# Kernel tuning notes

Measured on AMD Instinct MI355X. Metric: run time of the kernel, lower is better.

Reference implementation:

```python
import jax, jax.numpy as jnp
import numpy as np

D_MODEL = 768
N_HEADS = 12
CHUNK = 512
N_LM = 32
BATCH = 2
SEQ = 8192


def setup_inputs() -> dict:
    key = jax.random.key(0)
    ks = jax.random.split(key, 9)
    s = 1.0 / np.sqrt(D_MODEL)
    return {
        "x": jax.random.normal(ks[0], (BATCH, SEQ, D_MODEL), jnp.float32),
        "Wq": jax.random.normal(ks[1], (D_MODEL, D_MODEL), jnp.float32) * s,
        "bq": jax.random.normal(ks[2], (D_MODEL,), jnp.float32) * 0.01,
        "Wk": jax.random.normal(ks[3], (D_MODEL, D_MODEL), jnp.float32) * s,
        "bk": jax.random.normal(ks[4], (D_MODEL,), jnp.float32) * 0.01,
        "Wv": jax.random.normal(ks[5], (D_MODEL, D_MODEL), jnp.float32) * s,
        "bv": jax.random.normal(ks[6], (D_MODEL,), jnp.float32) * 0.01,
        "Wo": jax.random.normal(ks[7], (D_MODEL, D_MODEL), jnp.float32) * s,
        "bo": jax.random.normal(ks[8], (D_MODEL,), jnp.float32) * 0.01,
    }


def reference(x, Wq, bq, Wk, bk, Wv, bv, Wo, bo):
    B, S, D = x.shape
    H, hd = N_HEADS, D // N_HEADS
    scale = hd ** -0.5
    n_chunks = S // CHUNK  # SEQ chosen divisible by CHUNK -> no padding path

    # Global landmarks: mean-pool over N_LM evenly spaced segments
    seg = S // N_LM
    lm = x[:, : seg * N_LM, :].reshape(B, N_LM, seg, D).mean(axis=2)  # (B, L, D)

    # Q over local tokens only
    q = (x @ Wq.T + bq).reshape(B, n_chunks, CHUNK, H, hd)

    # K/V over [landmarks ++ local chunk]
    xc = x.reshape(B, n_chunks, CHUNK, D)
    lm_exp = jnp.broadcast_to(lm[:, None], (B, n_chunks, N_LM, D))
    kv = jnp.concatenate([lm_exp, xc], axis=2)  # (B, n_chunks, N_LM+CHUNK, D)
    k = (kv @ Wk.T + bk).reshape(B, n_chunks, N_LM + CHUNK, H, hd)
    v = (kv @ Wv.T + bv).reshape(B, n_chunks, N_LM + CHUNK, H, hd)

    attn = jnp.einsum("bnqhd,bnkhd->bnhqk", q, k) * scale
    attn = jax.nn.softmax(attn, axis=-1)  # dropout=0 (eval)
    out = jnp.einsum("bnhqk,bnkhd->bnqhd", attn, v).reshape(B, S, D)
    return out @ Wo.T + bo
```

## Files before the change

kernel.cpp:

```cpp
#include <hip/hip_runtime.h>
#include <cstdint>
#include <cstddef>

#define D_MODEL 768
#define N_HEADS 12
#define HEAD_DIM 64
#define CHUNK_SZ 512
#define N_LM 32
#define BATCH 2
#define SEQ 8192
#define N_CH 16
#define SEG 256
#define TOK (BATCH*SEQ)
#define MKV_PAD 16512
#define QSCALE 0.18033688011112042f
#define DEFER_THR 12.0f

typedef unsigned short u16;
typedef __attribute__((ext_vector_type(8))) __bf16 bf16x8;
typedef __attribute__((ext_vector_type(4))) float f32x4;

__device__ __forceinline__ u16 f2bf_rn(float f){
  union { __bf16 b; u16 u; } c; c.b = (__bf16)f; return c.u;
}

#define GLOAD_LDS16(gp, lp) \
  __builtin_amdgcn_global_load_lds((const __attribute__((address_space(1))) void*)(gp), \
                                   (__attribute__((address_space(3))) void*)(lp), 16, 0, 0)

__device__ __forceinline__ int xcd_remap(int bid, int nwg){
  int q = nwg >> 3, r = nwg & 7;
  int xcd = bid & 7, j = bid >> 3;
  return (xcd < r ? xcd*(q+1) : r*(q+1) + (xcd-r)*q) + j;
}

__global__ __launch_bounds__(256) void cvt4_kernel(
    const float* __restrict__ w0, const float* __restrict__ w1,
    const float* __restrict__ w2, const float* __restrict__ w3,
    u16* __restrict__ o0, u16* __restrict__ o1, u16* __restrict__ o2, u16* __restrict__ o3)
{
  const int n4 = D_MODEL*D_MODEL/4;
  int i = blockIdx.x*256 + threadIdx.x;
  int sel = i / n4, j = i - sel*n4;
  const float* s = sel==0 ? w0 : sel==1 ? w1 : sel==2 ? w2 : w3;
  u16* o = sel==0 ? o0 : sel==1 ? o1 : sel==2 ? o2 : o3;
  float4 v = reinterpret_cast<const float4*>(s)[j];
  ushort4 p; p.x=f2bf_rn(v.x); p.y=f2bf_rn(v.y); p.z=f2bf_rn(v.z); p.w=f2bf_rn(v.w);
  reinterpret_cast<ushort4*>(o)[j] = p;
}

__global__ void build_xcat_kernel(const float* __restrict__ x, u16* __restrict__ xcat){
  const int total4 = MKV_PAD * D_MODEL / 4;
  const int x4 = TOK * D_MODEL / 4;
  int stride = gridDim.x * blockDim.x;
  for (int i = blockIdx.x*blockDim.x + threadIdx.x; i < total4; i += stride){
    ushort4 o;
    if (i < x4){
      float4 v = reinterpret_cast<const float4*>(x)[i];
      o.x = f2bf_rn(v.x); o.y = f2bf_rn(v.y); o.z = f2bf_rn(v.z); o.w = f2bf_rn(v.w);
    } else { o.x = 0; o.y = 0; o.z = 0; o.w = 0; }
    reinterpret_cast<ushort4*>(xcat)[i] = o;
  }
}

__global__ __launch_bounds__(256) void lm_part_kernel(const float* __restrict__ x, float* __restrict__ lmp){
  int seg = blockIdx.x >> 3, sub = blockIdx.x & 7;
  int b = seg >> 5, l = seg & 31;
  const float* base = x + ((size_t)b*SEQ + (size_t)l*SEG + (size_t)sub*32) * D_MODEL;
  int d = threadIdx.x;
  float a0=0.f, a1=0.f, a2=0.f;
  for (int tt=0; tt<32; ++tt){
    const float* row = base + (size_t)tt*D_MODEL;
    a0 += row[d]; a1 += row[d+256]; a2 += row[d+512];
  }
  float* orow = lmp + (size_t)blockIdx.x * D_MODEL;
  orow[d] = a0; orow[d+256] = a1; orow[d+512] = a2;
}
__global__ __launch_bounds__(256) void lm_final_kernel(const float* __restrict__ lmp, u16* __restrict__ xcat){
  int seg = blockIdx.x;
  int d = threadIdx.x;
  float a0=0.f, a1=0.f, a2=0.f;
  #pragma unroll
  for (int i=0;i<8;i++){
    const float* p = lmp + ((size_t)seg*8 + i)*D_MODEL;
    a0 += p[d]; a1 += p[d+256]; a2 += p[d+512];
  }
  u16* orow = xcat + ((size_t)TOK + seg)*D_MODEL;
  const float inv = 1.f/(float)SEG;
  orow[d] = f2bf_rn(a0*inv); orow[d+256] = f2bf_rn(a1*inv); orow[d+512] = f2bf_rn(a2*inv);
}

#define GEMM_PROLOG                                                                \
  const int t = threadIdx.x;                                                       \
  const int lane = t & 63, wid = t >> 6;                                           \
  const int wr = wid >> 1, wc = wid & 1;                                           \
  const int lr = lane & 15, lg = lane >> 4;

#define GEMM_MAINLOOP(Aptr, Bptr)                                                  \
  __shared__ u16 As[128*64];                                                       \
  __shared__ u16 Bs[128*64];                                                       \
  const int srow = lane >> 3, scol = (lane & 7) << 3;                              \
  const u16* ga = (Aptr) + (row0 + srow)*(size_t)D_MODEL + scol;                   \
  const u16* gb = (Bptr) + ((size_t)col0 + srow)*(size_t)D_MODEL + scol;           \
  f32x4 acc[4][4];                                                                 \
  _Pragma("unroll") for (int m=0;m<4;m++)                                          \
    _Pragma("unroll") for (int n=0;n<4;n++) acc[m][n] = f32x4{0.f,0.f,0.f,0.f};    \
  for (int ko = 0; ko < D_MODEL; ko += 64){                                        \
    _Pragma("unroll") for (int i=0;i<4;i++){                                       \
      int chunk = wid*4 + i;                                                       \
      GLOAD_LDS16(ga + (size_t)chunk*8*D_MODEL + ko, As + chunk*512);              \
      GLOAD_LDS16(gb + (size_t)chunk*8*D_MODEL + ko, Bs + chunk*512);              \
    }                                                                              \
    __syncthreads();                                                               \
    _Pragma("unroll") for (int kk=0;kk<2;kk++){                                    \
      bf16x8 af[4], bv[4];                                                         \
      _Pragma("unroll") for (int m=0;m<4;m++)                                      \
        af[m] = *reinterpret_cast<const bf16x8*>(&As[(wr*64 + m*16 + lr)*64 + kk*32 + lg*8]); \
      _Pragma("unroll") for (int n=0;n<4;n++)                                      \
        bv[n] = *reinterpret_cast<const bf16x8*>(&Bs[(wc*64 + n*16 + lr)*64 + kk*32 + lg*8]); \
      _Pragma("unroll") for (int m=0;m<4;m++)                                      \
        _Pragma("unroll") for (int n=0;n<4;n++)                                    \
          acc[m][n] = __builtin_amdgcn_mfma_f32_16x16x32_bf16(af[m], bv[n], acc[m][n], 0, 0, 0); \
    }                                                                              \
    __syncthreads();                                                               \
  }

template<int OUT_F32, int BIAS_ROW, int ROWFAST, int NFAST>
__global__ __launch_bounds__(256) void gemm_bt_kernel(
    const u16* __restrict__ A, const u16* __restrict__ Bt,
    const float* __restrict__ bias, void* __restrict__ Cout, int ldc, float scale)
{
  int g = xcd_remap(blockIdx.x, gridDim.x);
  int rowt, colt;
  if (ROWFAST){ rowt = g % NFAST; colt = g / NFAST; }
  else        { colt = g % NFAST; rowt = g / NFAST; }
  const size_t row0 = (size_t)rowt * 128;
  const int col0 = colt * 128;
  GEMM_PROLOG
  GEMM_MAINLOOP(A, Bt)
  #pragma unroll
  for (int m=0;m<4;m++){
    #pragma unroll
    for (int n=0;n<4;n++){
      const int col = col0 + wc*64 + n*16 + lr;
      const float bcol = BIAS_ROW ? 0.f : bias[col];
      #pragma unroll
      for (int e=0;e<4;e++){
        size_t row = row0 + wr*64 + m*16 + lg*4 + e;
        float b = BIAS_ROW ? bias[row] : bcol;
        float val = (acc[m][n][e] + b) * scale;
        if (OUT_F32) reinterpret_cast<float*>(Cout)[row*(size_t)ldc + col] = val;
        else         reinterpret_cast<u16*>(Cout)[row*(size_t)ldc + col] = f2bf_rn(val);
      }
    }
  }
}

__global__ __launch_bounds__(256) void gemm_qk_kernel(
    const u16* __restrict__ A, const u16* __restrict__ Wqk,
    const float* __restrict__ bq, const float* __restrict__ bk,
    u16* __restrict__ Qb, u16* __restrict__ Kb)
{
  int g = xcd_remap(blockIdx.x, gridDim.x);
  int colt = g % 12, rowt = g / 12;
  const size_t row0 = (size_t)rowt * 128;
  const int col0 = colt * 128;
  GEMM_PROLOG
  GEMM_MAINLOOP(A, Wqk)
  const bool isk = col0 >= 768;
  const float scale = isk ? 1.f : QSCALE;
  u16* dst = isk ? Kb : Qb;
  #pragma unroll
  for (int m=0;m<4;m++){
    #pragma unroll
    for (int n=0;n<4;n++){
      const int col = col0 + wc*64 + n*16 + lr;
      const int ocol = isk ? col - 768 : col;
      const float b = isk ? bk[ocol] : bq[ocol];
      #pragma unroll
      for (int e=0;e<4;e++){
        size_t row = row0 + wr*64 + m*16 + lg*4 + e;
        if (isk || row < TOK){
          float val = (acc[m][n][e] + b) * scale;
          dst[row*D_MODEL + ocol] = f2bf_rn(val);
        }
      }
    }
  }
}

template<int NK>
__device__ __forceinline__ void attn_compute(
    int lr, int lg,
    const u16 (* __restrict__ Ks)[72], const u16 (* __restrict__ Vs)[72],
    u16 (* __restrict__ Pw)[72],
    const bf16x8 (&qf)[2][2], float (&m_run)[2], float (&l_run)[2], f32x4 (&of)[2][4])
{
  constexpr int NCF = NK/16;
  constexpr int NKT = NK/32;

  f32x4 s2[2][NCF];
  #pragma unroll
  for (int c=0;c<NCF;c++){
    bf16x8 kf0 = *reinterpret_cast<const bf16x8*>(&Ks[c*16 + lr][lg*8]);
    bf16x8 kf1 = *reinterpret_cast<const bf16x8*>(&Ks[c*16 + lr][32 + lg*8]);
    #pragma unroll
    for (int r=0;r<2;r++){
      f32x4 s = f32x4{0.f,0.f,0.f,0.f};
      s = __builtin_amdgcn_mfma_f32_16x16x32_bf16(kf0, qf[r][0], s, 0,0,0);
      s = __builtin_amdgcn_mfma_f32_16x16x32_bf16(kf1, qf[r][1], s, 0,0,0);
      s2[r][c] = s;
    }
  }

  bf16x8 vf[NKT][4];
  #pragma unroll
  for (int kt=0;kt<NKT;kt++)
    #pragma unroll
    for (int c=0;c<4;c++)
      vf[kt][c] = *reinterpret_cast<const bf16x8*>(&Vs[c*16 + lr][kt*32 + lg*8]);

  #pragma unroll
  for (int r=0;r<2;r++){
    float tm = s2[r][0][0];
    #pragma unroll
    for (int c=0;c<NCF;c++)
      #pragma unroll
      for (int e=0;e<4;e++) tm = fmaxf(tm, s2[r][c][e]);
    tm = fmaxf(tm, __shfl_xor(tm, 16, 64));
    tm = fmaxf(tm, __shfl_xor(tm, 32, 64));
    if (!__all(tm - m_run[r] <= DEFER_THR)){
      float mnew = fmaxf(m_run[r], tm);
      float al = exp2f(m_run[r] - mnew);
      m_run[r] = mnew;
      l_run[r] *= al;
      #pragma unroll
      for (int c=0;c<4;c++)
        #pragma unroll
        for (int e=0;e<4;e++) of[r][c][e] *= al;
    }
    float ts = 0.f;
    #pragma unroll
    for (int c=0;c<NCF;c++)
      #pragma unroll
      for (int e=0;e<4;e++){
        float p = exp2f(s2[r][c][e] - m_run[r]);
        s2[r][c][e] = p;
        ts += p;
      }
    ts += __shfl_xor(ts, 16, 64);
    ts += __shfl_xor(ts, 32, 64);
    l_run[r] += ts;

    #pragma unroll
    for (int c=0;c<NCF;c++){
      ushort4 pk;
      pk.x = f2bf_rn(s2[r][c][0]); pk.y = f2bf_rn(s2[r][c][1]);
      pk.z = f2bf_rn(s2[r][c][2]); pk.w = f2bf_rn(s2[r][c][3]);
      *reinterpret_cast<ushort4*>(&Pw[lr][c*16 + lg*4]) = pk;
    }
    #pragma unroll
    for (int kt=0;kt<NKT;kt++){
      bf16x8 pf = *reinterpret_cast<const bf16x8*>(&Pw[lr][kt*32 + lg*8]);
      #pragma unroll
      for (int c=0;c<4;c++)
        of[r][c] = __builtin_amdgcn_mfma_f32_16x16x32_bf16(vf[kt][c], pf, of[r][c], 0,0,0);
    }
  }
}

__global__ __launch_bounds__(256) void attn_kernel(
    const u16* __restrict__ Qb, const u16* __restrict__ Kb,
    const u16* __restrict__ Vt, u16* __restrict__ AO)
{
  __shared__ u16 Ks[64][72];
  __shared__ u16 Vs[64][72];
  __shared__ u16 PwAll[4][16][72];

  const int t = threadIdx.x;
  const int lane = t & 63, w = t >> 6;
  const int lr = lane & 15, lg = lane >> 4;
  const int qt = blockIdx.x;
  const int h  = blockIdx.y;
  const int b  = blockIdx.z >> 4, ch = blockIdx.z & 15;
  const size_t tok0 = (size_t)b*SEQ + (size_t)ch*CHUNK_SZ + (size_t)qt*128;
  const size_t bch0 = (size_t)b*SEQ + (size_t)ch*CHUNK_SZ;
  u16 (* __restrict__ Pw)[72] = PwAll[w];

  bf16x8 qf[2][2];
  #pragma unroll
  for (int r=0;r<2;r++)
    #pragma unroll
    for (int kk=0;kk<2;kk++)
      qf[r][kk] = *reinterpret_cast<const bf16x8*>(
          &Qb[(tok0 + w*32 + r*16 + lr)*D_MODEL + (size_t)h*HEAD_DIM + kk*32 + lg*8]);

  float m_run[2] = {-INFINITY, -INFINITY};
  float l_run[2] = {0.f, 0.f};
  f32x4 of[2][4];
  #pragma unroll
  for (int r=0;r<2;r++)
    #pragma unroll
    for (int c=0;c<4;c++) of[r][c] = f32x4{0.f,0.f,0.f,0.f};

  {
    const size_t lmrow0 = (size_t)TOK + (size_t)b*N_LM;
    int key = t >> 3, dc = (t & 7) << 3;
    *reinterpret_cast<bf16x8*>(&Ks[key][dc]) = *reinterpret_cast<const bf16x8*>(
        &Kb[(lmrow0 + key)*D_MODEL + (size_t)h*HEAD_DIM + dc]);
    int d = t >> 2, kc = (t & 3) << 3;
    *reinterpret_cast<bf16x8*>(&Vs[d][kc]) = *reinterpret_cast<const bf16x8*>(
        &Vt[((size_t)h*HEAD_DIM + d)*MKV_PAD + lmrow0 + kc]);
    __syncthreads();
    attn_compute<32>(lr, lg, Ks, Vs, Pw, qf, m_run, l_run, of);
  }

  bf16x8 kreg[2], vreg[2];
  const int key0 = t >> 3, dc0 = (t & 7) << 3;
  const int d0 = t >> 3, kc0 = (t & 7) << 3;
  {
    size_t col0 = bch0;
    kreg[0] = *reinterpret_cast<const bf16x8*>(&Kb[(col0 + key0)*D_MODEL + (size_t)h*HEAD_DIM + dc0]);
    kreg[1] = *reinterpret_cast<const bf16x8*>(&Kb[(col0 + key0 + 32)*D_MODEL + (size_t)h*HEAD_DIM + dc0]);
    vreg[0] = *reinterpret_cast<const bf16x8*>(&Vt[((size_t)h*HEAD_DIM + d0)*MKV_PAD + col0 + kc0]);
    vreg[1] = *reinterpret_cast<const bf16x8*>(&Vt[((size_t)h*HEAD_DIM + d0 + 32)*MKV_PAD + col0 + kc0]);
  }
  for (int tl = 0; tl < 8; ++tl){
    __syncthreads();
    *reinterpret_cast<bf16x8*>(&Ks[key0][dc0])      = kreg[0];
    *reinterpret_cast<bf16x8*>(&Ks[key0 + 32][dc0]) = kreg[1];
    *reinterpret_cast<bf16x8*>(&Vs[d0][kc0])        = vreg[0];
    *reinterpret_cast<bf16x8*>(&Vs[d0 + 32][kc0])   = vreg[1];
    __syncthreads();
    if (tl < 7){
      size_t col0 = bch0 + (size_t)(tl+1)*64;
      kreg[0] = *reinterpret_cast<const bf16x8*>(&Kb[(col0 + key0)*D_MODEL + (size_t)h*HEAD_DIM + dc0]);
      kreg[1] = *reinterpret_cast<const bf16x8*>(&Kb[(col0 + key0 + 32)*D_MODEL + (size_t)h*HEAD_DIM + dc0]);
      vreg[0] = *reinterpret_cast<const bf16x8*>(&Vt[((size_t)h*HEAD_DIM + d0)*MKV_PAD + col0 + kc0]);
      vreg[1] = *reinterpret_cast<const bf16x8*>(&Vt[((size_t)h*HEAD_DIM + d0 + 32)*MKV_PAD + col0 + kc0]);
    }
    attn_compute<64>(lr, lg, Ks, Vs, Pw, qf, m_run, l_run, of);
  }

  #pragma unroll
  for (int r=0;r<2;r++){
    float inv = 1.f / l_run[r];
    size_t row = (tok0 + w*32 + r*16 + lr)*D_MODEL + (size_t)h*HEAD_DIM;
    #pragma unroll
    for (int c=0;c<4;c++){
      ushort4 pk;
      pk.x = f2bf_rn(of[r][c][0]*inv); pk.y = f2bf_rn(of[r][c][1]*inv);
      pk.z = f2bf_rn(of[r][c][2]*inv); pk.w = f2bf_rn(of[r][c][3]*inv);
      *reinterpret_cast<ushort4*>(&AO[row + c*16 + lg*4]) = pk;
    }
  }
}

extern "C" void kernel_launch(void* const* d_in, const int* in_sizes, int n_in,
                              void* d_out, int out_size, void* d_ws, size_t ws_size,
                              hipStream_t stream) {
  const float* x  = (const float*)d_in[0];
  const float* Wq = (const float*)d_in[1];
  const float* bq = (const float*)d_in[2];
  const float* Wk = (const float*)d_in[3];
  const float* bk = (const float*)d_in[4];
  const float* Wv = (const float*)d_in[5];
  const float* bv = (const float*)d_in[6];
  const float* Wo = (const float*)d_in[7];
  const float* bo = (const float*)d_in[8];
  float* out = (float*)d_out;

  const size_t XCAT_OFF = 0;
  const size_t Q_OFF    = 25362432;
  const size_t K_OFF    = 50528256;
  const size_t VT_OFF   = 75890688;
  const size_t AO_OFF   = 101253120;
  const size_t WQ_OFF   = 126418944;
  const size_t WK_OFF   = 127598592;
  const size_t WV_OFF   = 128778240;
  const size_t WO_OFF   = 129957888;
  const size_t TOTAL    = 131137536;
  if (ws_size < TOTAL) return;

  char* ws = (char*)d_ws;
  u16* xcat = (u16*)(ws + XCAT_OFF);
  u16* Qb   = (u16*)(ws + Q_OFF);
  u16* Kb   = (u16*)(ws + K_OFF);
  u16* Vt   = (u16*)(ws + VT_OFF);
  u16* AO   = (u16*)(ws + AO_OFF);
  float* lmp = (float*)(ws + AO_OFF);
  u16* wqkb = (u16*)(ws + WQ_OFF);
  u16* wkb  = (u16*)(ws + WK_OFF);
  u16* wvb  = (u16*)(ws + WV_OFF);
  u16* wob  = (u16*)(ws + WO_OFF);

  dim3 blk(256);
  cvt4_kernel<<<dim3(2304), blk, 0, stream>>>(Wq, Wk, Wv, Wo, wqkb, wkb, wvb, wob);
  build_xcat_kernel<<<dim3(4096), blk, 0, stream>>>(x, xcat);
  lm_part_kernel<<<dim3(512), blk, 0, stream>>>(x, lmp);
  lm_final_kernel<<<dim3(64), blk, 0, stream>>>(lmp, xcat);

  gemm_qk_kernel<<<dim3(1548), blk, 0, stream>>>(xcat, wqkb, bq, bk, Qb, Kb);
  gemm_bt_kernel<0,1,1,6><<<dim3(774), blk, 0, stream>>>(wvb, xcat, bv, (void*)Vt, MKV_PAD, 1.f);

  attn_kernel<<<dim3(4, 12, 32), blk, 0, stream>>>(Qb, Kb, Vt, AO);

  gemm_bt_kernel<1,0,0,6><<<dim3(768), blk, 0, stream>>>(AO, wob, bo, (void*)out, D_MODEL, 1.f);
}
```

Before: 268.6 us.

## Double-buffer GEMM LDS tiles and XOR-swizzle columns to avoid bank conflicts

The shared GEMM main loop now uses two LDS buffers for the A and B tiles. It prefetches the next K-slice with direct global-to-LDS loads while MFMAs consume the current one, which removes one barrier per iteration. Global source columns are XOR-permuted by row and LDS reads apply the matching swizzle, so 16-byte fragment reads spread across banks. Doubling LDS to 64KB per block may reduce occupancy, and a single barrier per step relies on async load ordering.

```diff
diff --git a/kernel.cpp b/kernel.cpp
--- a/kernel.cpp
+++ b/kernel.cpp
@@ -97,32 +97,49 @@
   const int lr = lane & 15, lg = lane >> 4;
 
 #define GEMM_MAINLOOP(Aptr, Bptr)                                                  \
-  __shared__ u16 As[128*64];                                                       \
-  __shared__ u16 Bs[128*64];                                                       \
-  const int srow = lane >> 3, scol = (lane & 7) << 3;                              \
-  const u16* ga = (Aptr) + (row0 + srow)*(size_t)D_MODEL + scol;                   \
-  const u16* gb = (Bptr) + ((size_t)col0 + srow)*(size_t)D_MODEL + scol;           \
+  __shared__ u16 As[2*128*64];                                                     \
+  __shared__ u16 Bs[2*128*64];                                                     \
+  const int srow = lane >> 3;                                                      \
+  const int scolx = (((lane & 7) ^ (lane >> 3)) << 3);   \
+  const u16* ga = (Aptr) + (row0 + srow)*(size_t)D_MODEL + scolx;                  \
+  const u16* gb = (Bptr) + ((size_t)col0 + srow)*(size_t)D_MODEL + scolx;          \
   f32x4 acc[4][4];                                                                 \
   _Pragma("unroll") for (int m=0;m<4;m++)                                          \
     _Pragma("unroll") for (int n=0;n<4;n++) acc[m][n] = f32x4{0.f,0.f,0.f,0.f};    \
-  for (int ko = 0; ko < D_MODEL; ko += 64){                                        \
+  {                                                                                \
     _Pragma("unroll") for (int i=0;i<4;i++){                                       \
       int chunk = wid*4 + i;                                                       \
-      GLOAD_LDS16(ga + (size_t)chunk*8*D_MODEL + ko, As + chunk*512);              \
-      GLOAD_LDS16(gb + (size_t)chunk*8*D_MODEL + ko, Bs + chunk*512);              \
+      GLOAD_LDS16(ga + (size_t)chunk*8*D_MODEL, As + chunk*512);                   \
+      GLOAD_LDS16(gb + (size_t)chunk*8*D_MODEL, Bs + chunk*512);                   \
     }                                                                              \
-    __syncthreads();                                                               \
+  }                                                                                \
+  __syncthreads();                                                                 \
+  int cur = 0;                                                                     \
+  const int rsw = (lr & 7) << 3;                                                   \
+  for (int ts = 0; ts < D_MODEL/64; ++ts){                                         \
+    if (ts < D_MODEL/64 - 1){                                                      \
+      int nb = (cur ^ 1) * 8192;                                                   \
+      _Pragma("unroll") for (int i=0;i<4;i++){                                     \
+        int chunk = wid*4 + i;                                                     \
+        GLOAD_LDS16(ga + (size_t)chunk*8*D_MODEL + (ts+1)*64, As + nb + chunk*512);\
+        GLOAD_LDS16(gb + (size_t)chunk*8*D_MODEL + (ts+1)*64, Bs + nb + chunk*512);\
+      }                                                                            \
+    }                                                                              \
+    int cb = cur * 8192;                                                           \
     _Pragma("unroll") for (int kk=0;kk<2;kk++){                                    \
       bf16x8 af[4], bv[4];                                                         \
       _Pragma("unroll") for (int m=0;m<4;m++)                                      \
-        af[m] = *reinterpret_cast<const bf16x8*>(&As[(wr*64 + m*16 + lr)*64 + kk*32 + lg*8]); \
+        af[m] = *reinterpret_cast<const bf16x8*>(                                  \
+            &As[cb + (wr*64 + m*16 + lr)*64 + ((kk*32 + lg*8) ^ rsw)]);            \
       _Pragma("unroll") for (int n=0;n<4;n++)                                      \
-        bv[n] = *reinterpret_cast<const bf16x8*>(&Bs[(wc*64 + n*16 + lr)*64 + kk*32 + lg*8]); \
+        bv[n] = *reinterpret_cast<const bf16x8*>(                                  \
+            &Bs[cb + (wc*64 + n*16 + lr)*64 + ((kk*32 + lg*8) ^ rsw)]);            \
       _Pragma("unroll") for (int m=0;m<4;m++)                                      \
         _Pragma("unroll") for (int n=0;n<4;n++)                                    \
           acc[m][n] = __builtin_amdgcn_mfma_f32_16x16x32_bf16(af[m], bv[n], acc[m][n], 0, 0, 0); \
     }                                                                              \
     __syncthreads();                                                               \
+    cur ^= 1;                                                                      \
   }
 
 template<int OUT_F32, int BIAS_ROW, int ROWFAST, int NFAST>
```

Result: faster. 243.0 us (-9.5%).

## Restructure GEMMs: double-buffered swizzled LDS for one operand, direct global loads for other

Applied to the files above, without the earlier changes.

Replaces the shared GEMM main loop with a core that stages only one operand (the streamed activation tile) in double-buffered LDS, prefetching the next K-slice while computing the current one. The other operand (weights or the matching row block) is read directly from global memory into registers per wave. An XOR swizzle is applied to the LDS layout to avoid bank conflicts. This halves LDS traffic and removes one barrier per step, at the cost of uncoalesced-ish per-wave global fragment loads that rely on cache hits.

```diff
diff --git a/kernel.cpp b/kernel.cpp
--- a/kernel.cpp
+++ b/kernel.cpp
@@ -90,42 +90,63 @@
   orow[d] = f2bf_rn(a0*inv); orow[d+256] = f2bf_rn(a1*inv); orow[d+512] = f2bf_rn(a2*inv);
 }
 
+template<int SA>
+__device__ __forceinline__ void gemm_core(
+    const u16* __restrict__ Sg,
+    const u16* __restrict__ Rrow,
+    int wid, int lr, int lg, int shalf, f32x4 (&acc)[4][4])
+{
+  __shared__ u16 Sm[2*8192];
+  const int rsw = (lr & 7) << 3;
+  #pragma unroll
+  for (int i=0;i<4;i++){
+    int chunk = wid*4 + i;
+    GLOAD_LDS16(Sg + (size_t)chunk*8*D_MODEL, Sm + chunk*512);
+  }
+  __syncthreads();
+  int cur = 0;
+  for (int ts = 0; ts < D_MODEL/64; ++ts){
+    if (ts < D_MODEL/64 - 1){
+      int nb = (cur ^ 1) * 8192;
+      #pragma unroll
+      for (int i=0;i<4;i++){
+        int chunk = wid*4 + i;
+        GLOAD_LDS16(Sg + (size_t)chunk*8*D_MODEL + (ts+1)*64, Sm + nb + chunk*512);
+      }
+    }
+    const int cb = cur * 8192;
+    const int ko = ts * 64;
+    #pragma unroll
+    for (int kk=0;kk<2;kk++){
+      bf16x8 rf[4], lf[4];
+      #pragma unroll
+      for (int j=0;j<4;j++)
+        rf[j] = *reinterpret_cast<const bf16x8*>(Rrow + (size_t)j*16*D_MODEL + ko + kk*32 + lg*8);
+      #pragma unroll
+      for (int j=0;j<4;j++)
+        lf[j] = *reinterpret_cast<const bf16x8*>(
+            &Sm[cb + (shalf*64 + j*16 + lr)*64 + ((kk*32 + lg*8) ^ rsw)]);
+      #pragma unroll
+      for (int m=0;m<4;m++)
+        #pragma unroll
+        for (int n=0;n<4;n++)
+          acc[m][n] = __builtin_amdgcn_mfma_f32_16x16x32_bf16(
+              SA ? lf[m] : rf[m], SA ? rf[n] : lf[n], acc[m][n], 0, 0, 0);
+    }
+    __syncthreads();
+    cur ^= 1;
+  }
+}
+
 #define GEMM_PROLOG                                                                \
   const int t = threadIdx.x;                                                       \
   const int lane = t & 63, wid = t >> 6;                                           \
   const int wr = wid >> 1, wc = wid & 1;                                           \
-  const int lr = lane & 15, lg = lane >> 4;
-
-#define GEMM_MAINLOOP(Aptr, Bptr)                                                  \
-  __shared__ u16 As[128*64];                                                       \
-  __shared__ u16 Bs[128*64];                                                       \
-  const int srow = lane >> 3, scol = (lane & 7) << 3;                              \
-  const u16* ga = (Aptr) + (row0 + srow)*(size_t)D_MODEL + scol;                   \
-  const u16* gb = (Bptr) + ((size_t)col0 + srow)*(size_t)D_MODEL + scol;           \
-  f32x4 acc[4][4];                                                                 \
-  _Pragma("unroll") for (int m=0;m<4;m++)                                          \
-    _Pragma("unroll") for (int n=0;n<4;n++) acc[m][n] = f32x4{0.f,0.f,0.f,0.f};    \
-  for (int ko = 0; ko < D_MODEL; ko += 64){                                        \
-    _Pragma("unroll") for (int i=0;i<4;i++){                                       \
-      int chunk = wid*4 + i;                                                       \
-      GLOAD_LDS16(ga + (size_t)chunk*8*D_MODEL + ko, As + chunk*512);              \
-      GLOAD_LDS16(gb + (size_t)chunk*8*D_MODEL + ko, Bs + chunk*512);              \
-    }                                                                              \
-    __syncthreads();                                                               \
-    _Pragma("unroll") for (int kk=0;kk<2;kk++){                                    \
-      bf16x8 af[4], bv[4];                                                         \
-      _Pragma("unroll") for (int m=0;m<4;m++)                                      \
-        af[m] = *reinterpret_cast<const bf16x8*>(&As[(wr*64 + m*16 + lr)*64 + kk*32 + lg*8]); \
-      _Pragma("unroll") for (int n=0;n<4;n++)                                      \
-        bv[n] = *reinterpret_cast<const bf16x8*>(&Bs[(wc*64 + n*16 + lr)*64 + kk*32 + lg*8]); \
-      _Pragma("unroll") for (int m=0;m<4;m++)                                      \
-        _Pragma("unroll") for (int n=0;n<4;n++)                                    \
-          acc[m][n] = __builtin_amdgcn_mfma_f32_16x16x32_bf16(af[m], bv[n], acc[m][n], 0, 0, 0); \
-    }                                                                              \
-    __syncthreads();                                                               \
-  }
-
-template<int OUT_F32, int BIAS_ROW, int ROWFAST, int NFAST>
+  const int lr = lane & 15, lg = lane >> 4;                                        \
+  const int srow = lane >> 3;                                                      \
+  const int scolx = (((lane & 7) ^ (lane >> 3)) << 3);
+
+template<int OUT_F32, int BIAS_ROW, int ROWFAST, int NFAST, int SA>
 __global__ __launch_bounds__(256) void gemm_bt_kernel(
     const u16* __restrict__ A, const u16* __restrict__ Bt,
     const float* __restrict__ bias, void* __restrict__ Cout, int ldc, float scale)
@@ -137,7 +158,18 @@
   const size_t row0 = (size_t)rowt * 128;
   const int col0 = colt * 128;
   GEMM_PROLOG
-  GEMM_MAINLOOP(A, Bt)
+  f32x4 acc[4][4];
+  #pragma unroll
+  for (int m=0;m<4;m++)
+    #pragma unroll
+    for (int n=0;n<4;n++) acc[m][n] = f32x4{0.f,0.f,0.f,0.f};
+  if (SA){
+    gemm_core<1>(A + (row0 + srow)*(size_t)D_MODEL + scolx,
+                 Bt + ((size_t)col0 + wc*64 + lr)*D_MODEL, wid, lr, lg, wr, acc);
+  } else {
+    gemm_core<0>(Bt + ((size_t)col0 + srow)*(size_t)D_MODEL + scolx,
+                 A + (row0 + wr*64 + lr)*(size_t)D_MODEL, wid, lr, lg, wc, acc);
+  }
   #pragma unroll
   for (int m=0;m<4;m++){
     #pragma unroll
@@ -166,7 +198,13 @@
   const size_t row0 = (size_t)rowt * 128;
   const int col0 = colt * 128;
   GEMM_PROLOG
-  GEMM_MAINLOOP(A, Wqk)
+  f32x4 acc[4][4];
+  #pragma unroll
+  for (int m=0;m<4;m++)
+    #pragma unroll
+    for (int n=0;n<4;n++) acc[m][n] = f32x4{0.f,0.f,0.f,0.f};
+  gemm_core<1>(A + (row0 + srow)*(size_t)D_MODEL + scolx,
+               Wqk + ((size_t)col0 + wc*64 + lr)*D_MODEL, wid, lr, lg, wr, acc);
   const bool isk = col0 >= 768;
   const float scale = isk ? 1.f : QSCALE;
   u16* dst = isk ? Kb : Qb;
@@ -401,9 +439,9 @@
   lm_final_kernel<<<dim3(64), blk, 0, stream>>>(lmp, xcat);
 
   gemm_qk_kernel<<<dim3(1548), blk, 0, stream>>>(xcat, wqkb, bq, bk, Qb, Kb);
-  gemm_bt_kernel<0,1,1,6><<<dim3(774), blk, 0, stream>>>(wvb, xcat, bv, (void*)Vt, MKV_PAD, 1.f);
+  gemm_bt_kernel<0,1,1,6,0><<<dim3(774), blk, 0, stream>>>(wvb, xcat, bv, (void*)Vt, MKV_PAD, 1.f);
 
   attn_kernel<<<dim3(4, 12, 32), blk, 0, stream>>>(Qb, Kb, Vt, AO);
 
-  gemm_bt_kernel<1,0,0,6><<<dim3(768), blk, 0, stream>>>(AO, wob, bo, (void*)out, D_MODEL, 1.f);
-}
+  gemm_bt_kernel<1,0,0,6,1><<<dim3(768), blk, 0, stream>>>(AO, wob, bo, (void*)out, D_MODEL, 1.f);
+}
```

After: 304.4 us. 1.13x slower.
